# Kernel tuning notes

Hardware: AMD Instinct MI355X
Metric: run time of the kernel (lower is better)

The kernel has to match this reference:

```python
import jax, jax.numpy as jnp
import numpy as np

B, DIM, H, W = 8, 96, 256, 256
NH, WS, SS = 3, 8, 4
HD = DIM // NH
SCALE = HD ** -0.5
N = WS * WS  # tokens per window


def _rel_pos_log(ws):
    # [N, N, 2] signed log relative coordinates (matches get_relative_positions)
    coords = np.stack(np.meshgrid(np.arange(ws), np.arange(ws), indexing='ij'))
    cf = coords.reshape(2, -1)
    rel = (cf[:, :, None] - cf[:, None, :]).transpose(1, 2, 0).astype(np.float32)
    return np.sign(rel) * np.log1p(np.abs(rel))


def _attn_mask(Hh, Ww, ws, ss):
    # Swin shifted-window mask: [nW, N, N] with 0 / -100
    img = np.zeros((Hh, Ww))
    cnt = 0
    sl = (slice(0, -ws), slice(-ws, -ss), slice(-ss, None))
    for h in sl:
        for w in sl:
            img[h, w] = cnt
            cnt += 1
    mw = img.reshape(Hh // ws, ws, Ww // ws, ws).transpose(0, 2, 1, 3).reshape(-1, ws * ws)
    am = mw[:, None, :] - mw[:, :, None]
    return np.where(am != 0, -100.0, 0.0).astype(np.float32)


REL_POS = jnp.asarray(_rel_pos_log(WS))        # [N, N, 2]
ATTN_MASK = jnp.asarray(_attn_mask(H, W, WS, SS))  # [nW, N, N]


def setup_inputs() -> dict:
    key = jax.random.key(0)
    ks = jax.random.split(key, 8)
    s = 0.02
    return {
        'x': jax.random.normal(ks[0], (B, DIM, H, W), jnp.float32),
        'V_w': jax.random.normal(ks[1], (DIM, DIM), jnp.float32) * s,
        'V_b': jnp.zeros((DIM,), jnp.float32),
        'QK_w': jax.random.normal(ks[2], (2 * DIM, DIM), jnp.float32) * s,
        'QK_b': jnp.zeros((2 * DIM,), jnp.float32),
        'proj_w': jax.random.normal(ks[3], (DIM, DIM), jnp.float32) * s,
        'proj_b': jnp.zeros((DIM,), jnp.float32),
        'dw_w': jax.random.normal(ks[4], (DIM, 5, 5), jnp.float32) * s,
        'dw_b': jnp.zeros((DIM,), jnp.float32),
        'meta_w1': jax.random.normal(ks[5], (256, 2), jnp.float32) * 0.1,
        'meta_b1': jnp.zeros((256,), jnp.float32),
        'meta_w2': jax.random.normal(ks[6], (NH, 256), jnp.float32) * 0.1,
        'meta_b2': jnp.zeros((NH,), jnp.float32),
    }


def reference(x, V_w, V_b, QK_w, QK_b, proj_w, proj_b, dw_w, dw_b,
              meta_w1, meta_b1, meta_w2, meta_b2):
    # 1x1 convs as channel matmuls
    V = jnp.einsum('bchw,oc->bohw', x, V_w) + V_b[None, :, None, None]
    QK = jnp.einsum('bchw,oc->bohw', x, QK_w) + QK_b[None, :, None, None]
    qkv = jnp.concatenate([QK, V], axis=1).transpose(0, 2, 3, 1)  # [B,H,W,3C]
    # cyclic shift
    qkv = jnp.roll(qkv, (-SS, -SS), axis=(1, 2))
    # window partition -> [B*nW, N, 3C]
    xw = qkv.reshape(B, H // WS, WS, W // WS, WS, 3 * DIM)
    xw = xw.transpose(0, 1, 3, 2, 4, 5).reshape(-1, N, 3 * DIM)
    qkv3 = xw.reshape(-1, N, 3, NH, HD).transpose(2, 0, 3, 1, 4)  # [3, B_, nh, N, hd]
    q, k, v = qkv3[0] * SCALE, qkv3[1], qkv3[2]
    attn = jnp.einsum('whnd,whmd->whnm', q, k)  # [B_, nh, N, N]
    # MLP relative-position bias
    bias = jax.nn.relu(REL_POS @ meta_w1.T + meta_b1) @ meta_w2.T + meta_b2  # [N,N,nh]
    attn = attn + bias.transpose(2, 0, 1)[None]
    nW = ATTN_MASK.shape[0]
    attn = attn.reshape(B, nW, NH, N, N) + ATTN_MASK[None, :, None]
    attn = jax.nn.softmax(attn, axis=-1).reshape(-1, NH, N, N)
    xo = jnp.einsum('whnm,whmd->wnhd', attn, v).reshape(-1, N, DIM)
    # window reverse -> [B,H,W,C]
    xr = xo.reshape(B, H // WS, W // WS, WS, WS, DIM)
    xr = xr.transpose(0, 1, 3, 2, 4, 5).reshape(B, H, W, DIM)
    xr = jnp.roll(xr, (SS, SS), axis=(1, 2)).transpose(0, 3, 1, 2)  # [B,C,H,W]
    # depthwise 5x5 conv with reflect padding on V
    Vp = jnp.pad(V, ((0, 0), (0, 0), (2, 2), (2, 2)), mode='reflect')
    conv_out = jax.lax.conv_general_dilated(
        Vp, dw_w.reshape(DIM, 1, 5, 5), (1, 1), 'VALID',
        feature_group_count=DIM,
        dimension_numbers=('NCHW', 'OIHW', 'NCHW')) + dw_b[None, :, None, None]
    out = jnp.einsum('bchw,oc->bohw', conv_out + xr, proj_w) + proj_b[None, :, None, None]
    return out
```

## Files before the change

kernel.cpp:

```cpp
#include <hip/hip_runtime.h>
#include <hip/hip_bf16.h>

#define HW 65536
#define SCALE_Q 0.17677669529663687f

typedef __bf16 bf16x8 __attribute__((ext_vector_type(8)));
typedef float f32x4 __attribute__((ext_vector_type(4)));

__global__ void bias_kernel(const float* __restrict__ w1, const float* __restrict__ b1,
                            const float* __restrict__ w2, const float* __restrict__ b2,
                            float* __restrict__ biasF) {
    int gid = blockIdx.x * blockDim.x + threadIdx.x;
    if (gid >= 12288) return;
    int lane = gid & 63, r = (gid >> 6) & 3, ni = (gid >> 8) & 3, mi = (gid >> 10) & 3, h = gid >> 12;
    int i = mi * 16 + ((lane >> 4) << 2) + r;
    int j = ni * 16 + (lane & 15);
    float di = (float)((i >> 3) - (j >> 3));
    float dj = (float)((i & 7) - (j & 7));
    float r0 = (di > 0.f ? 1.f : (di < 0.f ? -1.f : 0.f)) * log1pf(fabsf(di));
    float r1 = (dj > 0.f ? 1.f : (dj < 0.f ? -1.f : 0.f)) * log1pf(fabsf(dj));
    float acc = 0.f;
    for (int t = 0; t < 256; ++t) {
        float u = fmaf(w1[2 * t], r0, fmaf(w1[2 * t + 1], r1, b1[t]));
        u = fmaxf(u, 0.f);
        acc = fmaf(w2[h * 256 + t], u, acc);
    }
    biasF[gid] = acc + b2[h];
}

__global__ void wtrans_kernel(const float* __restrict__ QK_w, const float* __restrict__ V_w,
                              const float* __restrict__ proj_w,
                              __bf16* __restrict__ Whi, __bf16* __restrict__ Wlo,
                              __bf16* __restrict__ WpHi, __bf16* __restrict__ WpLo) {
    int idx = blockIdx.x * blockDim.x + threadIdx.x;
    if (idx < 288 * 96) {
        int oo = idx / 96, c = idx - oo * 96;
        int h = oo / 96, rem = oo - h * 96, grp = rem >> 5, d = rem & 31;
        float w = (grp == 0) ? QK_w[(h * 32 + d) * 96 + c]
                : (grp == 1) ? QK_w[(96 + h * 32 + d) * 96 + c]
                             : V_w[(h * 32 + d) * 96 + c];
        __bf16 hi = (__bf16)w;
        Whi[idx] = hi;
        Wlo[idx] = (__bf16)(w - (float)hi);
    } else if (idx < 288 * 96 + 96 * 96) {
        int rdx = idx - 288 * 96;
        float w = proj_w[rdx];
        __bf16 hi = (__bf16)w;
        WpHi[rdx] = hi;
        WpLo[rdx] = (__bf16)(w - (float)hi);
    }
}

template <int MODE>
__global__ __launch_bounds__(256, 4) void fused_qkv_attn(
    const float* __restrict__ x,
    const __bf16* __restrict__ Whi, const __bf16* __restrict__ Wlo,
    const float* __restrict__ QK_b, const float* __restrict__ V_b,
    const float* __restrict__ biasF,
    unsigned short* __restrict__ Vout, void* __restrict__ xrv) {
    __shared__ __align__(16) char lds[39936];
    int tid = threadIdx.x;
    int w4 = tid >> 6;
    int lane = tid & 63;
    int l16 = lane & 15;
    int g8 = (lane >> 4) << 3;
    int g4 = (lane >> 4) << 2;
    int bx0 = blockIdx.x;
    int bxs = (bx0 & 7) * 256 + (bx0 >> 3);
    int b = bxs >> 8;
    int wh = (bxs >> 3) & 31;
    int ww0 = (bxs & 7) << 2;
    int wh8 = wh << 3;
    int ww = ww0 + w4;
    int wl = wh * 32 + ww;
    int ti = lane >> 3, tj = lane & 7;
    int ph = (wh8 + ti + 4) & 255;
    int pw = ((ww << 3) + tj + 4) & 255;
    int pos   = ph * 256 + pw;
    int pos_s = (wh8 + ti) * 256 + (ww << 3) + tj;

    const float* xb = x + (size_t)b * 96 * HW;
    bf16x8 Ah[4][3];
#pragma unroll
    for (int mi = 0; mi < 4; ++mi) {
        int t = mi * 16 + l16;
        int py = (wh8 + (t >> 3) + 4) & 255;
        int px = ((ww << 3) + (t & 7) + 4) & 255;
        const float* xp = xb + py * 256 + px + (size_t)g8 * HW;
#pragma unroll
        for (int ks = 0; ks < 3; ++ks)
#pragma unroll
            for (int e = 0; e < 8; ++e)
                Ah[mi][ks][e] = (__bf16)xp[(size_t)(ks * 32 + e) * HW];
    }

    char* hb = lds + w4 * 9984;
    __bf16* slab = (__bf16*)hb;
    __bf16* Vt   = (__bf16*)(hb + 5120);
    float*  Xr   = (float*)hb;

    bool bhh = (wh == 31), bww = (ww == 31);
    int rc[4];
#pragma unroll
    for (int ni = 0; ni < 4; ++ni) {
        int t = ni * 16 + l16;
        rc[ni] = (bhh ? (((t >> 3) < 4) ? 1 : 2) : 0) * 3 + (bww ? (((t & 7) < 4) ? 1 : 2) : 0);
    }

#pragma unroll 1
    for (int h = 0; h < 3; ++h) {
        bf16x8 Qf[4], Kf[4];
        {
            f32x4 acc[4][2];
#pragma unroll
            for (int mi = 0; mi < 4; ++mi)
#pragma unroll
                for (int ni = 0; ni < 2; ++ni) acc[mi][ni] = (f32x4){0.f, 0.f, 0.f, 0.f};
            __builtin_amdgcn_s_setprio(1);
#pragma unroll
            for (int ks = 0; ks < 3; ++ks)
#pragma unroll
                for (int ni = 0; ni < 2; ++ni) {
                    bf16x8 Bh = *(const bf16x8*)(Whi + (h * 96 + ni * 16 + l16) * 96 + ks * 32 + g8);
#pragma unroll
                    for (int mi = 0; mi < 4; ++mi)
                        acc[mi][ni] = __builtin_amdgcn_mfma_f32_16x16x32_bf16(Ah[mi][ks], Bh, acc[mi][ni], 0, 0, 0);
                }
            __builtin_amdgcn_s_setprio(0);
#pragma unroll
            for (int ni = 0; ni < 2; ++ni) {
                float bias = QK_b[h * 32 + ni * 16 + l16];
#pragma unroll
                for (int mi = 0; mi < 4; ++mi)
#pragma unroll
                    for (int r = 0; r < 4; ++r)
                        slab[(mi * 16 + g4 + r) * 40 + ni * 16 + l16] = (__bf16)((acc[mi][ni][r] + bias) * SCALE_Q);
            }
#pragma unroll
            for (int mi = 0; mi < 4; ++mi) Qf[mi] = *(const bf16x8*)(slab + (mi * 16 + l16) * 40 + g8);
        }
        {
            f32x4 acc[4][2];
#pragma unroll
            for (int mi = 0; mi < 4; ++mi)
#pragma unroll
                for (int ni = 0; ni < 2; ++ni) acc[mi][ni] = (f32x4){0.f, 0.f, 0.f, 0.f};
            __builtin_amdgcn_s_setprio(1);
#pragma unroll
            for (int ks = 0; ks < 3; ++ks)
#pragma unroll
                for (int ni = 0; ni < 2; ++ni) {
                    bf16x8 Bh = *(const bf16x8*)(Whi + (h * 96 + 32 + ni * 16 + l16) * 96 + ks * 32 + g8);
#pragma unroll
                    for (int mi = 0; mi < 4; ++mi)
                        acc[mi][ni] = __builtin_amdgcn_mfma_f32_16x16x32_bf16(Ah[mi][ks], Bh, acc[mi][ni], 0, 0, 0);
                }
            __builtin_amdgcn_s_setprio(0);
#pragma unroll
            for (int ni = 0; ni < 2; ++ni) {
                float bias = QK_b[96 + h * 32 + ni * 16 + l16];
#pragma unroll
                for (int mi = 0; mi < 4; ++mi)
#pragma unroll
                    for (int r = 0; r < 4; ++r)
                        slab[(mi * 16 + g4 + r) * 40 + ni * 16 + l16] = (__bf16)(acc[mi][ni][r] + bias);
            }
#pragma unroll
            for (int mi = 0; mi < 4; ++mi) Kf[mi] = *(const bf16x8*)(slab + (mi * 16 + l16) * 40 + g8);
        }
        {
            f32x4 acc[4][2];
#pragma unroll
            for (int mi = 0; mi < 4; ++mi)
#pragma unroll
                for (int ni = 0; ni < 2; ++ni) acc[mi][ni] = (f32x4){0.f, 0.f, 0.f, 0.f};
            __builtin_amdgcn_s_setprio(1);
#pragma unroll
            for (int ks = 0; ks < 3; ++ks)
#pragma unroll
                for (int ni = 0; ni < 2; ++ni) {
                    bf16x8 Bh = *(const bf16x8*)(Whi + (h * 96 + 64 + ni * 16 + l16) * 96 + ks * 32 + g8);
#pragma unroll
                    for (int mi = 0; mi < 4; ++mi)
                        acc[mi][ni] = __builtin_amdgcn_mfma_f32_16x16x32_bf16(Ah[mi][ks], Bh, acc[mi][ni], 0, 0, 0);
                }
            __builtin_amdgcn_s_setprio(0);
#pragma unroll
            for (int ni = 0; ni < 2; ++ni) {
                float bias = V_b[h * 32 + ni * 16 + l16];
#pragma unroll
                for (int mi = 0; mi < 4; ++mi)
#pragma unroll
                    for (int r = 0; r < 4; ++r)
                        Vt[(ni * 16 + l16) * 72 + mi * 16 + g4 + r] = (__bf16)(acc[mi][ni][r] + bias);
            }
        }
#pragma unroll
        for (int d = 0; d < 32; ++d)
            Vout[(size_t)(b * 96 + h * 32 + d) * HW + pos_s] = ((const unsigned short*)Vt)[d * 72 + lane];

        f32x4 sc[4][4];
        __builtin_amdgcn_s_setprio(1);
#pragma unroll
        for (int mi = 0; mi < 4; ++mi)
#pragma unroll
            for (int ni = 0; ni < 4; ++ni) {
                sc[mi][ni] = (f32x4){0.f, 0.f, 0.f, 0.f};
                sc[mi][ni] = __builtin_amdgcn_mfma_f32_16x16x32_bf16(Qf[mi], Kf[ni], sc[mi][ni], 0, 0, 0);
            }
        __builtin_amdgcn_s_setprio(0);
        const float* bF = biasF + h * 4096;
#pragma unroll
        for (int mi = 0; mi < 4; ++mi)
#pragma unroll
            for (int r = 0; r < 4; ++r) {
                int row = mi * 16 + g4 + r;
                float s0 = sc[mi][0][r] + bF[((mi * 4 + 0) * 4 + r) * 64 + lane];
                float s1 = sc[mi][1][r] + bF[((mi * 4 + 1) * 4 + r) * 64 + lane];
                float s2 = sc[mi][2][r] + bF[((mi * 4 + 2) * 4 + r) * 64 + lane];
                float s3 = sc[mi][3][r] + bF[((mi * 4 + 3) * 4 + r) * 64 + lane];
                if (bhh || bww) {
                    int rr = (bhh ? (((row >> 3) < 4) ? 1 : 2) : 0) * 3 +
                             (bww ? (((row & 7) < 4) ? 1 : 2) : 0);
                    if (rr != rc[0]) s0 -= 100.f;
                    if (rr != rc[1]) s1 -= 100.f;
                    if (rr != rc[2]) s2 -= 100.f;
                    if (rr != rc[3]) s3 -= 100.f;
                }
                float mm = fmaxf(fmaxf(s0, s1), fmaxf(s2, s3));
                mm = fmaxf(mm, __shfl_xor(mm, 1));
                mm = fmaxf(mm, __shfl_xor(mm, 2));
                mm = fmaxf(mm, __shfl_xor(mm, 4));
                mm = fmaxf(mm, __shfl_xor(mm, 8));
                float e0 = __expf(s0 - mm), e1 = __expf(s1 - mm);
                float e2 = __expf(s2 - mm), e3 = __expf(s3 - mm);
                float sum = e0 + e1 + e2 + e3;
                sum += __shfl_xor(sum, 1);
                sum += __shfl_xor(sum, 2);
                sum += __shfl_xor(sum, 4);
                sum += __shfl_xor(sum, 8);
                float inv = 1.f / sum;
                sc[mi][0][r] = e0 * inv;
                sc[mi][1][r] = e1 * inv;
                sc[mi][2][r] = e2 * inv;
                sc[mi][3][r] = e3 * inv;
            }
        f32x4 po[4][2];
#pragma unroll
        for (int mi = 0; mi < 4; ++mi)
#pragma unroll
            for (int ni = 0; ni < 2; ++ni) po[mi][ni] = (f32x4){0.f, 0.f, 0.f, 0.f};
#pragma unroll
        for (int ks = 0; ks < 2; ++ks) {
#pragma unroll
            for (int mi = 0; mi < 4; ++mi)
#pragma unroll
                for (int r = 0; r < 4; ++r) {
                    int row = mi * 16 + g4 + r;
                    slab[row * 40 + l16]      = (__bf16)sc[mi][ks * 2 + 0][r];
                    slab[row * 40 + 16 + l16] = (__bf16)sc[mi][ks * 2 + 1][r];
                }
            bf16x8 Vf[2], Pf;
#pragma unroll
            for (int ni = 0; ni < 2; ++ni)
                Vf[ni] = *(const bf16x8*)(Vt + (ni * 16 + l16) * 72 + ks * 32 + g8);
            __builtin_amdgcn_s_setprio(1);
#pragma unroll
            for (int mi = 0; mi < 4; ++mi) {
                Pf = *(const bf16x8*)(slab + (mi * 16 + l16) * 40 + g8);
#pragma unroll
                for (int ni = 0; ni < 2; ++ni)
                    po[mi][ni] = __builtin_amdgcn_mfma_f32_16x16x32_bf16(Pf, Vf[ni], po[mi][ni], 0, 0, 0);
            }
            __builtin_amdgcn_s_setprio(0);
        }
        if constexpr (MODE == 1) {
            __bf16* Xrt = slab;
#pragma unroll
            for (int mi = 0; mi < 4; ++mi)
#pragma unroll
                for (int ni = 0; ni < 2; ++ni)
#pragma unroll
                    for (int r = 0; r < 4; ++r)
                        Xrt[(ni * 16 + l16) * 72 + mi * 16 + g4 + r] = (__bf16)po[mi][ni][r];
            int d = lane >> 1, half = lane & 1;
            const unsigned short* src = (const unsigned short*)Xrt + d * 72 + half * 32;
            unsigned short* dst = (unsigned short*)xrv +
                ((size_t)(b * 96 + h * 32 + d) * 1024 + wl) * 64 + half * 32;
#pragma unroll
            for (int i = 0; i < 4; ++i)
                *(uint4*)(dst + i * 8) = *(const uint4*)(src + i * 8);
        } else {
#pragma unroll
            for (int mi = 0; mi < 4; ++mi)
#pragma unroll
                for (int ni = 0; ni < 2; ++ni)
#pragma unroll
                    for (int r = 0; r < 4; ++r)
                        Xr[(mi * 16 + g4 + r) * 36 + ni * 16 + l16] = po[mi][ni][r];
            float* xrg = (float*)xrv + (size_t)(b * 96 + h * 32) * HW + pos;
#pragma unroll
            for (int c4 = 0; c4 < 8; ++c4) {
                f32x4 v = *(const f32x4*)(Xr + lane * 36 + c4 * 4);
                xrg[(size_t)(c4 * 4 + 0) * HW] = v[0];
                xrg[(size_t)(c4 * 4 + 1) * HW] = v[1];
                xrg[(size_t)(c4 * 4 + 2) * HW] = v[2];
                xrg[(size_t)(c4 * 4 + 3) * HW] = v[3];
            }
        }
    }
}

template <int MODE>
__global__ __launch_bounds__(256) void dwproj_kernel(
    const __hip_bfloat16* __restrict__ Vs, const float* __restrict__ dw_w,
    const float* __restrict__ dw_b, const __bf16* __restrict__ WpHi,
    const __bf16* __restrict__ WpLo, const float* __restrict__ pb,
    const void* __restrict__ xrv, float* __restrict__ T) {
    __shared__ __align__(16) __bf16 Ts[13312];
    char* Tsb = (char*)Ts;
    int bx0 = blockIdx.x;
    int bx = (bx0 & 7) * 512 + (bx0 >> 3);
    int half = bx & 1, h = (bx >> 1) & 255, b = bx >> 9;
    int w0 = half << 7;
    int tid = threadIdx.x;
    for (int task = tid; task < 1536; task += 256) {
        int c = task >> 4, g = task & 15;
        int wbase = w0 + (g << 3);
        const __hip_bfloat16* Vp = Vs + (size_t)(b * 96 + c) * HW;
        const float* wt = dw_w + c * 25;
        float acc[8];
        float bias = dw_b[c];
#pragma unroll
        for (int i = 0; i < 8; ++i) acc[i] = bias;
        bool fast = (wbase >= 8) && (wbase <= 240);
#pragma unroll
        for (int dy = -2; dy <= 2; ++dy) {
            int hh = h + dy;
            hh = hh < 0 ? -hh : (hh > 255 ? 510 - hh : hh);
            int hs = (hh + 252) & 255;
            const __hip_bfloat16* row = Vp + hs * 256;
            float xv[12];
            if (fast) {
                const uint* rp = (const uint*)(row + (wbase - 6));
#pragma unroll
                for (int g2 = 0; g2 < 6; ++g2) {
                    uint u = rp[g2];
                    xv[2 * g2]     = __uint_as_float(u << 16);
                    xv[2 * g2 + 1] = __uint_as_float(u & 0xffff0000u);
                }
            } else {
#pragma unroll
                for (int idx = 0; idx < 12; ++idx) {
                    int cw = wbase - 2 + idx;
                    cw = cw < 0 ? -cw : (cw > 255 ? 510 - cw : cw);
                    int cs = (cw + 252) & 255;
                    uint u = *(const unsigned short*)(row + cs);
                    xv[idx] = __uint_as_float(u << 16);
                }
            }
            const float* w5 = wt + (dy + 2) * 5;
#pragma unroll
            for (int dx = 0; dx < 5; ++dx) {
                float wv = w5[dx];
#pragma unroll
                for (int i = 0; i < 8; ++i) acc[i] = fmaf(wv, xv[i + dx], acc[i]);
            }
        }
        if constexpr (MODE == 1) {
            int hs2 = (h + 252) & 255;
            int ps2 = (wbase + 252) & 255;
            int wrow = (hs2 >> 3) * 32;
            int rowoff = (hs2 & 7) * 8;
            const unsigned short* base = (const unsigned short*)xrv + (size_t)(b * 96 + c) * HW;
            uint2 A = *(const uint2*)(base + (size_t)(wrow + (ps2 >> 3)) * 64 + rowoff + 4);
            uint2 B = *(const uint2*)(base + (size_t)(wrow + (wbase >> 3)) * 64 + rowoff);
            acc[0] += __uint_as_float(A.x << 16);
            acc[1] += __uint_as_float(A.x & 0xffff0000u);
            acc[2] += __uint_as_float(A.y << 16);
            acc[3] += __uint_as_float(A.y & 0xffff0000u);
            acc[4] += __uint_as_float(B.x << 16);
            acc[5] += __uint_as_float(B.x & 0xffff0000u);
            acc[6] += __uint_as_float(B.y << 16);
            acc[7] += __uint_as_float(B.y & 0xffff0000u);
        } else {
            const float* xp = (const float*)xrv + (size_t)(b * 96 + c) * HW + h * 256;
            f32x4 x0 = *(const f32x4*)(xp + wbase);
            f32x4 x1 = *(const f32x4*)(xp + wbase + 4);
#pragma unroll
            for (int i = 0; i < 4; ++i) { acc[i] += x0[i]; acc[4 + i] += x1[i]; }
        }
#pragma unroll
        for (int i = 0; i < 8; ++i) {
            int px = g * 8 + i;
            *(__bf16*)(Tsb + (((px * 104 + c) * 2) ^ ((g & 7) << 4))) = (__bf16)acc[i];
        }
    }
    __syncthreads();
    int lane = tid & 63;
    int l16 = lane & 15;
    int g8 = (lane >> 4) << 3;
    int g4 = (lane >> 4) << 2;
    int wv = tid >> 6;
    f32x4 po[2][6];
#pragma unroll
    for (int mi = 0; mi < 2; ++mi)
#pragma unroll
        for (int ni = 0; ni < 6; ++ni) po[mi][ni] = (f32x4){0.f, 0.f, 0.f, 0.f};
#pragma unroll
    for (int ks = 0; ks < 3; ++ks) {
        bf16x8 Av[2];
#pragma unroll
        for (int mi = 0; mi < 2; ++mi) {
            int px = wv * 32 + mi * 16 + l16;
            Av[mi] = *(const bf16x8*)(Tsb + (((px * 104 + ks * 32 + g8) * 2) ^ (((px >> 3) & 7) << 4)));
        }
#pragma unroll
        for (int ni = 0; ni < 6; ++ni) {
            int o = ni * 16 + l16;
            bf16x8 Bh = *(const bf16x8*)(WpHi + o * 96 + ks * 32 + g8);
            bf16x8 Bl = *(const bf16x8*)(WpLo + o * 96 + ks * 32 + g8);
#pragma unroll
            for (int mi = 0; mi < 2; ++mi) {
                po[mi][ni] = __builtin_amdgcn_mfma_f32_16x16x32_bf16(Av[mi], Bh, po[mi][ni], 0, 0, 0);
                po[mi][ni] = __builtin_amdgcn_mfma_f32_16x16x32_bf16(Av[mi], Bl, po[mi][ni], 0, 0, 0);
            }
        }
    }
#pragma unroll
    for (int ni = 0; ni < 6; ++ni) {
        int o = ni * 16 + l16;
        float bias = pb[o];
#pragma unroll
        for (int mi = 0; mi < 2; ++mi) {
            f32x4 v = po[mi][ni];
            v[0] += bias; v[1] += bias; v[2] += bias; v[3] += bias;
            *(f32x4*)(T + (size_t)(b * 96 + o) * HW + h * 256 + w0 + wv * 32 + mi * 16 + g4) = v;
        }
    }
}

extern "C" void kernel_launch(void* const* d_in, const int* in_sizes, int n_in,
                              void* d_out, int out_size, void* d_ws, size_t ws_size,
                              hipStream_t stream) {
    const float* x      = (const float*)d_in[0];
    const float* V_w    = (const float*)d_in[1];
    const float* V_b    = (const float*)d_in[2];
    const float* QK_w   = (const float*)d_in[3];
    const float* QK_b   = (const float*)d_in[4];
    const float* proj_w = (const float*)d_in[5];
    const float* proj_b = (const float*)d_in[6];
    const float* dw_w   = (const float*)d_in[7];
    const float* dw_b   = (const float*)d_in[8];
    const float* mw1    = (const float*)d_in[9];
    const float* mb1    = (const float*)d_in[10];
    const float* mw2    = (const float*)d_in[11];
    const float* mb2    = (const float*)d_in[12];
    float* out = (float*)d_out;

    char* ws = (char*)d_ws;
    const size_t VB = 100663296;
    const size_t TAB = 49152 + 2 * 55296 + 2 * 18432;
    int mode = (ws_size >= 2 * VB + TAB) ? 1 : 0;

    __hip_bfloat16* Vbuf = (__hip_bfloat16*)ws;
    size_t off = VB;
    unsigned short* xr16 = nullptr;
    if (mode == 1) { xr16 = (unsigned short*)(ws + off); off += VB; }
    float*  biasF = (float*)(ws + off); off += 49152;
    __bf16* Whi   = (__bf16*)(ws + off); off += 55296;
    __bf16* Wlo   = (__bf16*)(ws + off); off += 55296;
    __bf16* WpHi  = (__bf16*)(ws + off); off += 18432;
    __bf16* WpLo  = (__bf16*)(ws + off);

    bias_kernel<<<48, 256, 0, stream>>>(mw1, mb1, mw2, mb2, biasF);
    wtrans_kernel<<<144, 256, 0, stream>>>(QK_w, V_w, proj_w, Whi, Wlo, WpHi, WpLo);
    if (mode == 1) {
        fused_qkv_attn<1><<<2048, 256, 0, stream>>>(x, Whi, Wlo, QK_b, V_b, biasF,
                                                    (unsigned short*)Vbuf, (void*)xr16);
        dwproj_kernel<1><<<4096, 256, 0, stream>>>(Vbuf, dw_w, dw_b, WpHi, WpLo, proj_b,
                                                   (const void*)xr16, out);
    } else {
        fused_qkv_attn<0><<<2048, 256, 0, stream>>>(x, Whi, Wlo, QK_b, V_b, biasF,
                                                    (unsigned short*)Vbuf, (void*)out);
        dwproj_kernel<0><<<4096, 256, 0, stream>>>(Vbuf, dw_w, dw_b, WpHi, WpLo, proj_b,
                                                   (const void*)out, out);
    }
}
```

Measured before the change: 646.6 us.

## Store V in window-major bf16 layout with vectorized writes and reads

The attention kernel now writes V per window as contiguous 64-element rows using 16-byte stores, replacing 32 scattered 2-byte stores per lane. The depthwise conv kernel reads V from this window-major layout, with two 16-byte loads per row on the fast path. An empty asm barrier is also added to pin the A fragments in registers. The aim is to cut uncoalesced global write traffic, at the cost of more complex indexing and scattered loads on the boundary path.

```diff
diff --git a/kernel.cpp b/kernel.cpp
--- a/kernel.cpp
+++ b/kernel.cpp
@@ -76,8 +76,7 @@
     int ti = lane >> 3, tj = lane & 7;
     int ph = (wh8 + ti + 4) & 255;
     int pw = ((ww << 3) + tj + 4) & 255;
-    int pos   = ph * 256 + pw;
-    int pos_s = (wh8 + ti) * 256 + (ww << 3) + tj;
+    int pos = ph * 256 + pw;
 
     const float* xb = x + (size_t)b * 96 * HW;
     bf16x8 Ah[4][3];
@@ -93,6 +92,13 @@
             for (int e = 0; e < 8; ++e)
                 Ah[mi][ks][e] = (__bf16)xp[(size_t)(ks * 32 + e) * HW];
     }
+#pragma unroll
+    for (int mi = 0; mi < 4; ++mi)
+#pragma unroll
+        for (int ks = 0; ks < 3; ++ks) {
+            f32x4* ap = (f32x4*)&Ah[mi][ks];
+            asm volatile("" : "+v"(*ap));
+        }
 
     char* hb = lds + w4 * 9984;
     __bf16* slab = (__bf16*)hb;
@@ -106,6 +112,7 @@
         int t = ni * 16 + l16;
         rc[ni] = (bhh ? (((t >> 3) < 4) ? 1 : 2) : 0) * 3 + (bww ? (((t & 7) < 4) ? 1 : 2) : 0);
     }
+    int d2 = lane >> 1, hf = lane & 1;
 
 #pragma unroll 1
     for (int h = 0; h < 3; ++h) {
@@ -195,9 +202,13 @@
                         Vt[(ni * 16 + l16) * 72 + mi * 16 + g4 + r] = (__bf16)(acc[mi][ni][r] + bias);
             }
         }
-#pragma unroll
-        for (int d = 0; d < 32; ++d)
-            Vout[(size_t)(b * 96 + h * 32 + d) * HW + pos_s] = ((const unsigned short*)Vt)[d * 72 + lane];
+        {
+            const unsigned short* srcV = (const unsigned short*)Vt + d2 * 72 + hf * 32;
+            unsigned short* dstV = Vout + ((size_t)(b * 96 + h * 32 + d2) * 1024 + wl) * 64 + hf * 32;
+#pragma unroll
+            for (int i = 0; i < 4; ++i)
+                *(uint4*)(dstV + i * 8) = *(const uint4*)(srcV + i * 8);
+        }
 
         f32x4 sc[4][4];
         __builtin_amdgcn_s_setprio(1);
@@ -283,10 +294,9 @@
 #pragma unroll
                     for (int r = 0; r < 4; ++r)
                         Xrt[(ni * 16 + l16) * 72 + mi * 16 + g4 + r] = (__bf16)po[mi][ni][r];
-            int d = lane >> 1, half = lane & 1;
-            const unsigned short* src = (const unsigned short*)Xrt + d * 72 + half * 32;
+            const unsigned short* src = (const unsigned short*)Xrt + d2 * 72 + hf * 32;
             unsigned short* dst = (unsigned short*)xrv +
-                ((size_t)(b * 96 + h * 32 + d) * 1024 + wl) * 64 + half * 32;
+                ((size_t)(b * 96 + h * 32 + d2) * 1024 + wl) * 64 + hf * 32;
 #pragma unroll
             for (int i = 0; i < 4; ++i)
                 *(uint4*)(dst + i * 8) = *(const uint4*)(src + i * 8);
@@ -313,7 +323,7 @@
 
 template <int MODE>
 __global__ __launch_bounds__(256) void dwproj_kernel(
-    const __hip_bfloat16* __restrict__ Vs, const float* __restrict__ dw_w,
+    const unsigned short* __restrict__ Vw, const float* __restrict__ dw_w,
     const float* __restrict__ dw_b, const __bf16* __restrict__ WpHi,
     const __bf16* __restrict__ WpLo, const float* __restrict__ pb,
     const void* __restrict__ xrv, float* __restrict__ T) {
@@ -327,35 +337,44 @@
     for (int task = tid; task < 1536; task += 256) {
         int c = task >> 4, g = task & 15;
         int wbase = w0 + (g << 3);
-        const __hip_bfloat16* Vp = Vs + (size_t)(b * 96 + c) * HW;
+        const unsigned short* Vp = Vw + (size_t)(b * 96 + c) * HW;
         const float* wt = dw_w + c * 25;
         float acc[8];
         float bias = dw_b[c];
 #pragma unroll
         for (int i = 0; i < 8; ++i) acc[i] = bias;
         bool fast = (wbase >= 8) && (wbase <= 240);
+        int kwin = wbase >> 3;
 #pragma unroll
         for (int dy = -2; dy <= 2; ++dy) {
             int hh = h + dy;
             hh = hh < 0 ? -hh : (hh > 255 ? 510 - hh : hh);
             int hs = (hh + 252) & 255;
-            const __hip_bfloat16* row = Vp + hs * 256;
+            int wrow = (hs >> 3) << 5;
+            int rowoff = (hs & 7) << 3;
             float xv[12];
             if (fast) {
-                const uint* rp = (const uint*)(row + (wbase - 6));
-#pragma unroll
-                for (int g2 = 0; g2 < 6; ++g2) {
-                    uint u = rp[g2];
-                    xv[2 * g2]     = __uint_as_float(u << 16);
-                    xv[2 * g2 + 1] = __uint_as_float(u & 0xffff0000u);
-                }
+                uint4 A = *(const uint4*)(Vp + (size_t)(wrow + kwin - 1) * 64 + rowoff);
+                uint4 Bv = *(const uint4*)(Vp + (size_t)(wrow + kwin) * 64 + rowoff);
+                xv[0]  = __uint_as_float(A.y << 16);
+                xv[1]  = __uint_as_float(A.y & 0xffff0000u);
+                xv[2]  = __uint_as_float(A.z << 16);
+                xv[3]  = __uint_as_float(A.z & 0xffff0000u);
+                xv[4]  = __uint_as_float(A.w << 16);
+                xv[5]  = __uint_as_float(A.w & 0xffff0000u);
+                xv[6]  = __uint_as_float(Bv.x << 16);
+                xv[7]  = __uint_as_float(Bv.x & 0xffff0000u);
+                xv[8]  = __uint_as_float(Bv.y << 16);
+                xv[9]  = __uint_as_float(Bv.y & 0xffff0000u);
+                xv[10] = __uint_as_float(Bv.z << 16);
+                xv[11] = __uint_as_float(Bv.z & 0xffff0000u);
             } else {
 #pragma unroll
                 for (int idx = 0; idx < 12; ++idx) {
                     int cw = wbase - 2 + idx;
                     cw = cw < 0 ? -cw : (cw > 255 ? 510 - cw : cw);
                     int cs = (cw + 252) & 255;
-                    uint u = *(const unsigned short*)(row + cs);
+                    uint u = Vp[(size_t)(wrow + (cs >> 3)) * 64 + rowoff + (cs & 7)];
                     xv[idx] = __uint_as_float(u << 16);
                 }
             }
@@ -370,11 +389,11 @@
         if constexpr (MODE == 1) {
             int hs2 = (h + 252) & 255;
             int ps2 = (wbase + 252) & 255;
-            int wrow = (hs2 >> 3) * 32;
-            int rowoff = (hs2 & 7) * 8;
+            int wrow2 = (hs2 >> 3) * 32;
+            int rowoff2 = (hs2 & 7) * 8;
             const unsigned short* base = (const unsigned short*)xrv + (size_t)(b * 96 + c) * HW;
-            uint2 A = *(const uint2*)(base + (size_t)(wrow + (ps2 >> 3)) * 64 + rowoff + 4);
-            uint2 B = *(const uint2*)(base + (size_t)(wrow + (wbase >> 3)) * 64 + rowoff);
+            uint2 A = *(const uint2*)(base + (size_t)(wrow2 + (ps2 >> 3)) * 64 + rowoff2 + 4);
+            uint2 B = *(const uint2*)(base + (size_t)(wrow2 + (wbase >> 3)) * 64 + rowoff2);
             acc[0] += __uint_as_float(A.x << 16);
             acc[1] += __uint_as_float(A.x & 0xffff0000u);
             acc[2] += __uint_as_float(A.y << 16);
@@ -463,7 +482,7 @@
     const size_t TAB = 49152 + 2 * 55296 + 2 * 18432;
     int mode = (ws_size >= 2 * VB + TAB) ? 1 : 0;
 
-    __hip_bfloat16* Vbuf = (__hip_bfloat16*)ws;
+    unsigned short* Vbuf = (unsigned short*)ws;
     size_t off = VB;
     unsigned short* xr16 = nullptr;
     if (mode == 1) { xr16 = (unsigned short*)(ws + off); off += VB; }
@@ -477,12 +496,12 @@
     wtrans_kernel<<<144, 256, 0, stream>>>(QK_w, V_w, proj_w, Whi, Wlo, WpHi, WpLo);
     if (mode == 1) {
         fused_qkv_attn<1><<<2048, 256, 0, stream>>>(x, Whi, Wlo, QK_b, V_b, biasF,
-                                                    (unsigned short*)Vbuf, (void*)xr16);
+                                                    Vbuf, (void*)xr16);
         dwproj_kernel<1><<<4096, 256, 0, stream>>>(Vbuf, dw_w, dw_b, WpHi, WpLo, proj_b,
                                                    (const void*)xr16, out);
     } else {
         fused_qkv_attn<0><<<2048, 256, 0, stream>>>(x, Whi, Wlo, QK_b, V_b, biasF,
-                                                    (unsigned short*)Vbuf, (void*)out);
+                                                    Vbuf, (void*)out);
         dwproj_kernel<0><<<4096, 256, 0, stream>>>(Vbuf, dw_w, dw_b, WpHi, WpLo, proj_b,
                                                    (const void*)out, out);
     }
```

Result: slower. 672.0 us (+3.9%).
